# Optimization experiments

Hardware: AMD Instinct MI355X
Metric: run time of the kernel (lower is better)

Reference implementation:

```python
import jax, jax.numpy as jnp
import numpy as np

B, N, F, T = 32, 2048, 16, 64


def setup_inputs() -> dict:
    key = jax.random.key(0)
    ks = jax.random.split(key, 6)
    return {
        "x": jax.random.normal(ks[0], (B, N, F, T), dtype=jnp.float32),
        "U1": jax.random.normal(ks[1], (N, 1), dtype=jnp.float32) * (1.0 / np.sqrt(N)),
        "U2": jax.random.normal(ks[2], (F, N), dtype=jnp.float32) * (1.0 / np.sqrt(F)),
        "U3": jax.random.normal(ks[3], (1, F), dtype=jnp.float32) * (1.0 / np.sqrt(F)),
        "be": jax.random.normal(ks[4], (1, T, T), dtype=jnp.float32),
        "Ve": jax.random.normal(ks[5], (T, T), dtype=jnp.float32) * (1.0 / np.sqrt(T)),
    }


def reference(x, U1, U2, U3, be, Ve):
    # x: (B, N, F, T)
    # lhs = squeeze(x^T(0,3,2,1) @ U1) @ U2 : contract N then project F->N -> (B, T, N)
    lhs = jnp.einsum("bnft,n->btf", x, U1[:, 0]) @ U2  # (B, T, N)
    # rhs = squeeze(U3 @ x, -2): contract F -> (B, N, T)
    rhs = jnp.einsum("f,bnft->bnt", U3[0], x)  # (B, N, T)
    product = jnp.matmul(lhs, rhs)  # (B, T, T)
    E = jnp.einsum("ts,bsu->btu", Ve, jax.nn.sigmoid(product + be))  # (B, T, T)
    return jax.nn.softmax(E, axis=1)
```

## Files before the change

### kernel.cpp

```cpp
#include <hip/hip_runtime.h>
#include <hip/hip_bf16.h>
#include <math.h>


#define B_ 32
#define N_ 2048
#define F_ 16
#define T_ 64
#define NPB 64
#define CHUNKS (N_ / NPB)

__global__ __launch_bounds__(256) void ta_pass1(
    const float* __restrict__ x, const float* __restrict__ U1,
    const float* __restrict__ U2, const float* __restrict__ U3,
    float* __restrict__ partial)
{
  const int blk    = blockIdx.x;
  const int b      = blk / CHUNKS;
  const int chunk  = blk % CHUNKS;
  const int n_base = chunk * NPB;
  const int tid    = threadIdx.x;
  const int tp     = tid & 15;
  const int n_sub  = tid >> 4;
  const int w      = tid >> 6;
  const int lane   = tid & 63;

  __shared__ float  u1s[NPB];
  __shared__ float  u2t[NPB][F_ + 1];
  __shared__ float4 rlds[NPB][16];
  __shared__ float4 red[4][256];

  if (tid < NPB) u1s[tid] = U1[n_base + tid];
  for (int i = tid; i < NPB * F_; i += 256) {
    const int f = i >> 6, n = i & 63;
    u2t[n][f] = U2[f * N_ + n_base + n];
  }
  float u3r[F_];
  #pragma unroll
  for (int f = 0; f < F_; ++f) u3r[f] = U3[f];
  __syncthreads();

  float4 ya[F_];
  #pragma unroll
  for (int f = 0; f < F_; ++f) ya[f] = make_float4(0.f, 0.f, 0.f, 0.f);

  const float* xb = x + ((size_t)b * N_ + n_base) * (F_ * T_);
  #pragma unroll
  for (int it = 0; it < NPB / 16; ++it) {
    const int nl = n_sub + it * 16;
    const float* xn = xb + (size_t)nl * (F_ * T_) + 4 * tp;
    const float u1 = u1s[nl];
    float4 r = make_float4(0.f, 0.f, 0.f, 0.f);
    #pragma unroll
    for (int f = 0; f < F_; ++f) {
      const float4 v = *reinterpret_cast<const float4*>(xn + f * T_);
      ya[f].x = fmaf(u1, v.x, ya[f].x);
      ya[f].y = fmaf(u1, v.y, ya[f].y);
      ya[f].z = fmaf(u1, v.z, ya[f].z);
      ya[f].w = fmaf(u1, v.w, ya[f].w);
      r.x = fmaf(u3r[f], v.x, r.x);
      r.y = fmaf(u3r[f], v.y, r.y);
      r.z = fmaf(u3r[f], v.z, r.z);
      r.w = fmaf(u3r[f], v.w, r.w);
    }
    rlds[nl][tp] = r;
  }

  #pragma unroll
  for (int f = 0; f < F_; ++f) {
    ya[f].x += __shfl_xor(ya[f].x, 16);
    ya[f].y += __shfl_xor(ya[f].y, 16);
    ya[f].z += __shfl_xor(ya[f].z, 16);
    ya[f].w += __shfl_xor(ya[f].w, 16);
    ya[f].x += __shfl_xor(ya[f].x, 32);
    ya[f].y += __shfl_xor(ya[f].y, 32);
    ya[f].z += __shfl_xor(ya[f].z, 32);
    ya[f].w += __shfl_xor(ya[f].w, 32);
  }
  if ((lane >> 4) == 0) {
    #pragma unroll
    for (int f = 0; f < F_; ++f) red[w][f * 16 + tp] = ya[f];
  }
  __syncthreads();

  float4* pb = reinterpret_cast<float4*>(partial + (size_t)blk * 2048);
  {
    const float4 a = red[0][tid], c = red[1][tid], d = red[2][tid], e = red[3][tid];
    float4 yv;
    yv.x = a.x + c.x + d.x + e.x;
    yv.y = a.y + c.y + d.y + e.y;
    yv.z = a.z + c.z + d.z + e.z;
    yv.w = a.w + c.w + d.w + e.w;
    pb[tid] = yv;
  }
  {
    const int f = tid >> 4, uq = tid & 15;
    float4 zv = make_float4(0.f, 0.f, 0.f, 0.f);
    #pragma unroll
    for (int n = 0; n < NPB; ++n) {
      const float  u2 = u2t[n][f];
      const float4 r  = rlds[n][uq];
      zv.x = fmaf(u2, r.x, zv.x);
      zv.y = fmaf(u2, r.y, zv.y);
      zv.z = fmaf(u2, r.z, zv.z);
      zv.w = fmaf(u2, r.w, zv.w);
    }
    pb[256 + tid] = zv;
  }
}

__global__ __launch_bounds__(256) void ta_finish(
    const float* __restrict__ partial, const float* __restrict__ be,
    const float* __restrict__ Ve, float* __restrict__ out)
{
  const int b   = blockIdx.x;
  const int tid = threadIdx.x;
  __shared__ float ys[T_][F_ + 1];
  __shared__ float zs[F_][T_];
  __shared__ float sig[T_][T_ + 1];
  __shared__ float Es[T_][T_ + 1];

  const float4* p4 = reinterpret_cast<const float4*>(partial) + (size_t)b * CHUNKS * 512;
  #pragma unroll
  for (int k = 0; k < 2; ++k) {
    const int i4 = tid + k * 256;
    float4 s = make_float4(0.f, 0.f, 0.f, 0.f);
    #pragma unroll 4
    for (int j = 0; j < CHUNKS; ++j) {
      const float4 v = p4[(size_t)j * 512 + i4];
      s.x += v.x; s.y += v.y; s.z += v.z; s.w += v.w;
    }
    if (i4 < 256) {
      const int f = i4 >> 4, t0 = (i4 & 15) * 4;
      ys[t0 + 0][f] = s.x; ys[t0 + 1][f] = s.y;
      ys[t0 + 2][f] = s.z; ys[t0 + 3][f] = s.w;
    } else {
      const int j4 = i4 - 256;
      const int f = j4 >> 4, u0 = (j4 & 15) * 4;
      zs[f][u0 + 0] = s.x; zs[f][u0 + 1] = s.y;
      zs[f][u0 + 2] = s.z; zs[f][u0 + 3] = s.w;
    }
  }
  __syncthreads();

  const int tr = tid >> 2;
  const int ub = (tid & 3) * 16;
  #pragma unroll
  for (int i = 0; i < 16; ++i) {
    const int u = ub + i;
    float acc = 0.f;
    #pragma unroll
    for (int f = 0; f < F_; ++f) acc = fmaf(ys[tr][f], zs[f][u], acc);
    acc += be[tr * T_ + u];
    sig[tr][u] = 1.f / (1.f + __expf(-acc));
  }
  __syncthreads();
  #pragma unroll
  for (int i = 0; i < 16; ++i) {
    const int u = ub + i;
    float acc = 0.f;
    #pragma unroll
    for (int s = 0; s < T_; ++s) acc = fmaf(Ve[tr * T_ + s], sig[s][u], acc);
    Es[tr][u] = acc;
  }
  __syncthreads();

  const int u = tid >> 2, p = tid & 3;
  float m = -INFINITY;
  #pragma unroll
  for (int r = 0; r < 16; ++r) m = fmaxf(m, Es[p * 16 + r][u]);
  m = fmaxf(m, __shfl_xor(m, 1));
  m = fmaxf(m, __shfl_xor(m, 2));
  float den = 0.f;
  #pragma unroll
  for (int r = 0; r < 16; ++r) den += __expf(Es[p * 16 + r][u] - m);
  den += __shfl_xor(den, 1);
  den += __shfl_xor(den, 2);
  const float inv = 1.f / den;
  #pragma unroll
  for (int r = 0; r < 16; ++r)
    out[(size_t)b * T_ * T_ + (p * 16 + r) * T_ + u] =
        __expf(Es[p * 16 + r][u] - m) * inv;
}

extern "C" void kernel_launch(void* const* d_in, const int* in_sizes, int n_in,
                              void* d_out, int out_size, void* d_ws, size_t ws_size,
                              hipStream_t stream) {
  const float* x  = (const float*)d_in[0];
  const float* U1 = (const float*)d_in[1];
  const float* U2 = (const float*)d_in[2];
  const float* U3 = (const float*)d_in[3];
  const float* be = (const float*)d_in[4];
  const float* Ve = (const float*)d_in[5];
  float* out = (float*)d_out;
  float* partial = (float*)d_ws;

  ta_pass1<<<B_ * CHUNKS, 256, 0, stream>>>(x, U1, U2, U3, partial);
  ta_finish<<<B_, 256, 0, stream>>>(partial, be, Ve, out);
}
```

Measured before the change: 77.17 us.

## Remap pass1 threads so each thread owns one (f,t-quad) and shuffle-reduce over F

Each thread now handles a single float4 of x per n row, indexed by its tid, instead of looping over all 16 features. The U1 contraction therefore needs only one float4 accumulator with no cross-thread reduction. The U3 contraction over F is done with warp shuffles on every row, and the U2 projection is accumulated in registers using U2 values packed as float4 in shared memory. This cuts register pressure enough to request 6 blocks per CU and removes the rlds staging buffer. The cost is eight shuffles per row and different global load coalescing.

```diff
diff --git a/kernel.cpp b/kernel.cpp
--- a/kernel.cpp
+++ b/kernel.cpp
@@ -10,7 +10,7 @@
 #define NPB 64
 #define CHUNKS (N_ / NPB)
 
-__global__ __launch_bounds__(256) void ta_pass1(
+__global__ __launch_bounds__(256, 6) void ta_pass1(
     const float* __restrict__ x, const float* __restrict__ U1,
     const float* __restrict__ U2, const float* __restrict__ U3,
     float* __restrict__ partial)
@@ -20,93 +20,68 @@
   const int chunk  = blk % CHUNKS;
   const int n_base = chunk * NPB;
   const int tid    = threadIdx.x;
-  const int tp     = tid & 15;
-  const int n_sub  = tid >> 4;
+  const int lane   = tid & 63;
   const int w      = tid >> 6;
-  const int lane   = tid & 63;
+  const int g      = lane >> 4;
+  const int tq     = lane & 15;
 
-  __shared__ float  u1s[NPB];
-  __shared__ float  u2t[NPB][F_ + 1];
-  __shared__ float4 rlds[NPB][16];
-  __shared__ float4 red[4][256];
+  __shared__ float4 u2q[NPB][4];
+  __shared__ float4 zred[4][256];
 
-  if (tid < NPB) u1s[tid] = U1[n_base + tid];
   for (int i = tid; i < NPB * F_; i += 256) {
     const int f = i >> 6, n = i & 63;
-    u2t[n][f] = U2[f * N_ + n_base + n];
+    reinterpret_cast<float*>(&u2q[n][f & 3])[f >> 2] = U2[f * N_ + n_base + n];
   }
-  float u3r[F_];
-  #pragma unroll
-  for (int f = 0; f < F_; ++f) u3r[f] = U3[f];
+  const float u3own = U3[tid >> 4];
   __syncthreads();
 
-  float4 ya[F_];
-  #pragma unroll
-  for (int f = 0; f < F_; ++f) ya[f] = make_float4(0.f, 0.f, 0.f, 0.f);
+  float4 ya  = make_float4(0.f, 0.f, 0.f, 0.f);
+  float4 za0 = ya, za1 = ya, za2 = ya, za3 = ya;
 
-  const float* xb = x + ((size_t)b * N_ + n_base) * (F_ * T_);
-  #pragma unroll
-  for (int it = 0; it < NPB / 16; ++it) {
-    const int nl = n_sub + it * 16;
-    const float* xn = xb + (size_t)nl * (F_ * T_) + 4 * tp;
-    const float u1 = u1s[nl];
-    float4 r = make_float4(0.f, 0.f, 0.f, 0.f);
-    #pragma unroll
-    for (int f = 0; f < F_; ++f) {
-      const float4 v = *reinterpret_cast<const float4*>(xn + f * T_);
-      ya[f].x = fmaf(u1, v.x, ya[f].x);
-      ya[f].y = fmaf(u1, v.y, ya[f].y);
-      ya[f].z = fmaf(u1, v.z, ya[f].z);
-      ya[f].w = fmaf(u1, v.w, ya[f].w);
-      r.x = fmaf(u3r[f], v.x, r.x);
-      r.y = fmaf(u3r[f], v.y, r.y);
-      r.z = fmaf(u3r[f], v.z, r.z);
-      r.w = fmaf(u3r[f], v.w, r.w);
-    }
-    rlds[nl][tp] = r;
+  const float4* xb = reinterpret_cast<const float4*>(x)
+                   + ((size_t)b * N_ + n_base) * 256;
+  #pragma unroll 4
+  for (int n = 0; n < NPB; ++n) {
+    const float4 v  = xb[n * 256 + tid];
+    const float  u1 = U1[n_base + n];
+    ya.x = fmaf(u1, v.x, ya.x);
+    ya.y = fmaf(u1, v.y, ya.y);
+    ya.z = fmaf(u1, v.z, ya.z);
+    ya.w = fmaf(u1, v.w, ya.w);
+    float4 rp;
+    rp.x = u3own * v.x; rp.y = u3own * v.y;
+    rp.z = u3own * v.z; rp.w = u3own * v.w;
+    rp.x += __shfl_xor(rp.x, 16); rp.y += __shfl_xor(rp.y, 16);
+    rp.z += __shfl_xor(rp.z, 16); rp.w += __shfl_xor(rp.w, 16);
+    rp.x += __shfl_xor(rp.x, 32); rp.y += __shfl_xor(rp.y, 32);
+    rp.z += __shfl_xor(rp.z, 32); rp.w += __shfl_xor(rp.w, 32);
+    const float4 u2v = u2q[n][g];
+    za0.x = fmaf(u2v.x, rp.x, za0.x); za0.y = fmaf(u2v.x, rp.y, za0.y);
+    za0.z = fmaf(u2v.x, rp.z, za0.z); za0.w = fmaf(u2v.x, rp.w, za0.w);
+    za1.x = fmaf(u2v.y, rp.x, za1.x); za1.y = fmaf(u2v.y, rp.y, za1.y);
+    za1.z = fmaf(u2v.y, rp.z, za1.z); za1.w = fmaf(u2v.y, rp.w, za1.w);
+    za2.x = fmaf(u2v.z, rp.x, za2.x); za2.y = fmaf(u2v.z, rp.y, za2.y);
+    za2.z = fmaf(u2v.z, rp.z, za2.z); za2.w = fmaf(u2v.z, rp.w, za2.w);
+    za3.x = fmaf(u2v.w, rp.x, za3.x); za3.y = fmaf(u2v.w, rp.y, za3.y);
+    za3.z = fmaf(u2v.w, rp.z, za3.z); za3.w = fmaf(u2v.w, rp.w, za3.w);
   }
 
-  #pragma unroll
-  for (int f = 0; f < F_; ++f) {
-    ya[f].x += __shfl_xor(ya[f].x, 16);
-    ya[f].y += __shfl_xor(ya[f].y, 16);
-    ya[f].z += __shfl_xor(ya[f].z, 16);
-    ya[f].w += __shfl_xor(ya[f].w, 16);
-    ya[f].x += __shfl_xor(ya[f].x, 32);
-    ya[f].y += __shfl_xor(ya[f].y, 32);
-    ya[f].z += __shfl_xor(ya[f].z, 32);
-    ya[f].w += __shfl_xor(ya[f].w, 32);
-  }
-  if ((lane >> 4) == 0) {
-    #pragma unroll
-    for (int f = 0; f < F_; ++f) red[w][f * 16 + tp] = ya[f];
-  }
+  zred[w][(g +  0) * 16 + tq] = za0;
+  zred[w][(g +  4) * 16 + tq] = za1;
+  zred[w][(g +  8) * 16 + tq] = za2;
+  zred[w][(g + 12) * 16 + tq] = za3;
   __syncthreads();
 
   float4* pb = reinterpret_cast<float4*>(partial + (size_t)blk * 2048);
-  {
-    const float4 a = red[0][tid], c = red[1][tid], d = red[2][tid], e = red[3][tid];
-    float4 yv;
-    yv.x = a.x + c.x + d.x + e.x;
-    yv.y = a.y + c.y + d.y + e.y;
-    yv.z = a.z + c.z + d.z + e.z;
-    yv.w = a.w + c.w + d.w + e.w;
-    pb[tid] = yv;
-  }
-  {
-    const int f = tid >> 4, uq = tid & 15;
-    float4 zv = make_float4(0.f, 0.f, 0.f, 0.f);
-    #pragma unroll
-    for (int n = 0; n < NPB; ++n) {
-      const float  u2 = u2t[n][f];
-      const float4 r  = rlds[n][uq];
-      zv.x = fmaf(u2, r.x, zv.x);
-      zv.y = fmaf(u2, r.y, zv.y);
-      zv.z = fmaf(u2, r.z, zv.z);
-      zv.w = fmaf(u2, r.w, zv.w);
-    }
-    pb[256 + tid] = zv;
-  }
+  pb[tid] = ya;
+  const float4 a0 = zred[0][tid], a1 = zred[1][tid];
+  const float4 a2 = zred[2][tid], a3 = zred[3][tid];
+  float4 zv;
+  zv.x = a0.x + a1.x + a2.x + a3.x;
+  zv.y = a0.y + a1.y + a2.y + a3.y;
+  zv.z = a0.z + a1.z + a2.z + a3.z;
+  zv.w = a0.w + a1.w + a2.w + a3.w;
+  pb[256 + tid] = zv;
 }
 
 __global__ __launch_bounds__(256) void ta_finish(
```

New measurement: 79.45 us. +3.0%, slower.
